# Performance work log

Measured on AMD Instinct MI355X. Metric: run time of the kernel, lower is better.

The kernel has to match this reference:

```python
import jax, jax.numpy as jnp
import numpy as np

EPS = 1e-12  # torch F.normalize default eps

def _l2norm(x, axis=-1):
    n = jnp.sqrt(jnp.sum(x * x, axis=axis, keepdims=True))
    return x / jnp.maximum(n, EPS)

def setup_inputs() -> dict:
    key = jax.random.key(0)
    k1, k2, k3 = jax.random.split(key, 3)
    B, L, D, C, J = 16, 1024, 768, 500, 10
    spatial = jax.random.normal(k1, (B, L, D), dtype=jnp.float32)
    prototypes = jax.random.normal(k2, (C, J, D), dtype=jnp.float32) * 0.02
    raw_weights = jnp.full((C, J), -2.0, dtype=jnp.float32) + 0.1 * jax.random.normal(k3, (C, J), dtype=jnp.float32)
    bias = jnp.zeros((C,), dtype=jnp.float32)
    return {"spatial": spatial, "prototypes": prototypes, "raw_weights": raw_weights, "bias": bias}

def reference(spatial, prototypes, raw_weights, bias):
    # spatial: (B, L, D); prototypes: (C, J, D)
    z = _l2norm(spatial)            # (B, L, D)
    p = _l2norm(prototypes)         # (C, J, D)
    sim = jnp.einsum('bld,cjd->blcj', z, p)   # (B, L, C, J)
    pooled = jnp.max(sim, axis=1)              # (B, C, J) max over L
    weights = jax.nn.softplus(raw_weights)     # (C, J)
    logits = jnp.sum(pooled * weights[None], axis=-1) + bias  # (B, C)
    return logits
```

## Files before the change

### kernel.cpp

```cpp
#include <hip/hip_runtime.h>

#define B_     16
#define L_     1024
#define D_     768
#define C_     500
#define J_     10
#define M_     (B_ * L_)
#define NREAL  (C_ * J_)
#define NPAD   5120
#define TM     256
#define TN     256
#define TK     64
#define KTILES (D_ / TK)

typedef __attribute__((ext_vector_type(8))) short short8;
typedef __attribute__((ext_vector_type(4))) float f32x4;

struct frag2 { short8 k[2]; };

static __device__ __forceinline__ unsigned f2ord(float f) {
    unsigned u = __float_as_uint(f);
    return (u & 0x80000000u) ? ~u : (u | 0x80000000u);
}
static __device__ __forceinline__ float ord2f(unsigned u) {
    return (u & 0x80000000u) ? __uint_as_float(u & 0x7fffffffu)
                             : __uint_as_float(~u);
}

static __device__ __forceinline__ unsigned short f2bf(float f) {
    unsigned u = __float_as_uint(f);
    u += 0x7fffu + ((u >> 16) & 1u);
    return (unsigned short)(u >> 16);
}

__global__ __launch_bounds__(256) void prep_kernel(
    const float* __restrict__ spatial, const float* __restrict__ protos,
    unsigned short* __restrict__ z, unsigned short* __restrict__ pbuf,
    unsigned int* __restrict__ pooled)
{
    const int bid = blockIdx.x;
    if (bid < 80) {
        uint4 zz = {0, 0, 0, 0};
        *(uint4*)(pooled + bid * 1024 + threadIdx.x * 4) = zz;
    }

    const float* in;
    unsigned short* out;
    int row, valid;
    if (bid < 4096) { in = spatial; out = z;    row = bid * 4 + (threadIdx.x >> 6);          valid = M_; }
    else            { in = protos;  out = pbuf; row = (bid - 4096) * 4 + (threadIdx.x >> 6); valid = NREAL; }
    const int lane = threadIdx.x & 63;

    unsigned short* orow = out + (size_t)row * D_;
    if (row >= valid) {
        ushort4 zz = {0, 0, 0, 0};
        #pragma unroll
        for (int p = 0; p < 3; ++p)
            *(ushort4*)(orow + (p * 64 + lane) * 4) = zz;
        return;
    }

    const float4* rp = (const float4*)(in + (size_t)row * D_);
    float4 v[3];
    float s = 0.f;
    #pragma unroll
    for (int p = 0; p < 3; ++p) {
        v[p] = rp[p * 64 + lane];
        s += v[p].x * v[p].x + v[p].y * v[p].y + v[p].z * v[p].z + v[p].w * v[p].w;
    }
    #pragma unroll
    for (int off = 32; off; off >>= 1) s += __shfl_xor(s, off);
    float inv = 1.f / fmaxf(sqrtf(s), 1e-12f);
    #pragma unroll
    for (int p = 0; p < 3; ++p) {
        ushort4 o;
        o.x = f2bf(v[p].x * inv);
        o.y = f2bf(v[p].y * inv);
        o.z = f2bf(v[p].z * inv);
        o.w = f2bf(v[p].w * inv);
        *(ushort4*)(orow + (p * 64 + lane) * 4) = o;
    }
}


#define MFMA(a, b, c) __builtin_amdgcn_mfma_f32_16x16x32_bf16(a, b, c, 0, 0, 0)
#define FENCE asm volatile("" ::: "memory")
#define BAR   do { FENCE; __builtin_amdgcn_s_barrier(); FENCE; } while (0)
#define VM(N) asm volatile("s_waitcnt vmcnt(" #N ")" ::: "memory")
#define PRIO1 __builtin_amdgcn_s_setprio(1)
#define PRIO0 __builtin_amdgcn_s_setprio(0)

#define RD_A2(dst, p, mi) do { \
    dst[0].k[0] = *(const short8*)(bA0 + (p)*32768 + (mi)*1024); \
    dst[0].k[1] = *(const short8*)(bA1 + (p)*32768 + (mi)*1024); \
    dst[1].k[0] = *(const short8*)(bA0 + (p)*32768 + ((mi)+1)*1024); \
    dst[1].k[1] = *(const short8*)(bA1 + (p)*32768 + ((mi)+1)*1024); \
} while (0)

#define RD_B4(dst, p) do { \
    _Pragma("unroll") \
    for (int ni_ = 0; ni_ < 4; ++ni_) { \
        dst[ni_].k[0] = *(const short8*)(bB0 + (p)*32768 + ni_*1024); \
        dst[ni_].k[1] = *(const short8*)(bB1 + (p)*32768 + ni_*1024); \
    } \
} while (0)

#define STAGE_A(p, q, k0) __builtin_amdgcn_global_load_lds( \
    (const __attribute__((address_space(1))) void*)(Z + gA0 + (q)*64*D_ + (unsigned)(k0)), \
    (__attribute__((address_space(3))) void*)(lds + (p)*32768 + (q)*4096 + tid8), 16, 0, 0)
#define STAGE_B(p, q, k0) __builtin_amdgcn_global_load_lds( \
    (const __attribute__((address_space(1))) void*)(Pm + gB0 + (q)*64*D_ + (unsigned)(k0)), \
    (__attribute__((address_space(3))) void*)(lds + (p)*32768 + 16384 + (q)*4096 + tid8), 16, 0, 0)

#define MMPAIR(j, S, Bv) do { \
    PRIO1; \
    _Pragma("unroll") \
    for (int ni_ = 0; ni_ < 4; ++ni_) { \
        acc[2*(j)][ni_]   = MFMA(S[0].k[0], Bv[ni_].k[0], acc[2*(j)][ni_]); \
        acc[2*(j)+1][ni_] = MFMA(S[1].k[0], Bv[ni_].k[0], acc[2*(j)+1][ni_]); \
        acc[2*(j)][ni_]   = MFMA(S[0].k[1], Bv[ni_].k[1], acc[2*(j)][ni_]); \
        acc[2*(j)+1][ni_] = MFMA(S[1].k[1], Bv[ni_].k[1], acc[2*(j)+1][ni_]); \
    } \
    PRIO0; \
} while (0)

__global__ __launch_bounds__(512, 1) void gemm_maxpool_kernel(
    const unsigned short* __restrict__ Z,
    const unsigned short* __restrict__ Pm,
    unsigned int* __restrict__ pooled)
{
    __shared__ unsigned short lds[65536];

    const int tid  = threadIdx.x;
    const int lane = tid & 63;
    const int wid  = tid >> 6;
    const int wm   = wid >> 2;
    const int wn   = wid & 3;

    const int xcd = (int)blockIdx.x & 7;
    const int idx = (int)blockIdx.x >> 3;
    const int bm  = xcd * 8 + (idx & 7);
    const int bn  = idx >> 3;
    const int row0 = bm * TM;
    const int col0 = bn * TN;

    const int tr    = tid >> 3;
    const int tswz  = ((tid & 7) * 16) ^ ((tr & 7) << 4);
    const int tid8  = tid * 8;
    const unsigned gA0 = (unsigned)(row0 + tr) * D_ + (tswz >> 1);
    const unsigned gB0 = (unsigned)(col0 + tr) * D_ + (tswz >> 1);

    const int l15   = lane & 15;
    const int swzl  = (lane & 7) << 4;
    const int colS0 = ((((lane >> 4) * 16)      ) ^ swzl) >> 1;
    const int colS1 = ((((lane >> 4) * 16) + 64 ) ^ swzl) >> 1;
    const unsigned short* bA0 = lds + (wm * 128 + l15) * 64 + colS0;
    const unsigned short* bA1 = lds + (wm * 128 + l15) * 64 + colS1;
    const unsigned short* bB0 = lds + 16384 + (wn * 64 + l15) * 64 + colS0;
    const unsigned short* bB1 = lds + 16384 + (wn * 64 + l15) * 64 + colS1;

    f32x4 acc[8][4] = {};
    frag2 aE[2], aO[2], bE[4], bO[4];

    STAGE_B(0,0,0);  STAGE_B(0,1,0);  STAGE_A(0,0,0);  STAGE_A(0,2,0);
    STAGE_B(0,2,0);  STAGE_B(0,3,0);  STAGE_A(0,1,0);  STAGE_A(0,3,0);
    STAGE_B(1,0,64); STAGE_B(1,1,64); STAGE_A(1,0,64); STAGE_A(1,2,64);
    STAGE_B(1,2,64); STAGE_B(1,3,64); STAGE_A(1,1,64); STAGE_A(1,3,64);
    VM(8);
    BAR;
    RD_B4(bE, 0);
    RD_A2(aE, 0, 0);

    #pragma unroll 1
    for (int i = 0; i < 5; ++i) {
        const int kE = i * 128 + 128;
        const int kO = i * 128 + 192;
        frag2 t23[2], t45[2], t67[2];

        RD_A2(t23, 0, 2);  STAGE_B(0, 0, kE);  STAGE_B(0, 1, kE);
        BAR; MMPAIR(0, aE, bE); BAR;

        RD_A2(t45, 0, 4);  STAGE_A(0, 0, kE);  STAGE_A(0, 2, kE);
        BAR; MMPAIR(1, t23, bE); BAR;

        RD_A2(t67, 0, 6);  STAGE_B(0, 2, kE);  STAGE_B(0, 3, kE);
        VM(6);
        BAR; MMPAIR(2, t45, bE); BAR;

        STAGE_A(0, 1, kE);  STAGE_A(0, 3, kE);
        MMPAIR(3, t67, bE);
        RD_B4(bO, 1);  RD_A2(aO, 1, 0);
        BAR;

        RD_A2(t23, 1, 2);  STAGE_B(1, 0, kO);  STAGE_B(1, 1, kO);
        BAR; MMPAIR(0, aO, bO); BAR;

        RD_A2(t45, 1, 4);  STAGE_A(1, 0, kO);  STAGE_A(1, 2, kO);
        BAR; MMPAIR(1, t23, bO); BAR;

        RD_A2(t67, 1, 6);  STAGE_B(1, 2, kO);  STAGE_B(1, 3, kO);
        VM(6);
        BAR; MMPAIR(2, t45, bO); BAR;

        STAGE_A(1, 1, kO);  STAGE_A(1, 3, kO);
        MMPAIR(3, t67, bO);
        RD_B4(bE, 0);  RD_A2(aE, 0, 0);
        BAR;
    }

    {
        frag2 t23[2], t45[2], t67[2];
        RD_A2(t23, 0, 2);
        BAR; MMPAIR(0, aE, bE); BAR;
        RD_A2(t45, 0, 4);
        BAR; MMPAIR(1, t23, bE); BAR;
        RD_A2(t67, 0, 6);
        VM(0);
        BAR; MMPAIR(2, t45, bE); BAR;
        MMPAIR(3, t67, bE);
        RD_B4(bO, 1);  RD_A2(aO, 1, 0);
        BAR;

        RD_A2(t23, 1, 2);
        BAR; MMPAIR(0, aO, bO); BAR;
        RD_A2(t45, 1, 4);
        BAR; MMPAIR(1, t23, bO); BAR;
        RD_A2(t67, 1, 6);
        BAR; MMPAIR(2, t45, bO); BAR;
        MMPAIR(3, t67, bO);
    }

    const int batch = row0 >> 10;
    #pragma unroll
    for (int ni = 0; ni < 4; ++ni) {
        float v = -3.0e38f;
        #pragma unroll
        for (int mi = 0; mi < 8; ++mi)
            v = fmaxf(v, fmaxf(fmaxf(acc[mi][ni][0], acc[mi][ni][1]),
                               fmaxf(acc[mi][ni][2], acc[mi][ni][3])));
        v = fmaxf(v, __shfl_xor(v, 16));
        v = fmaxf(v, __shfl_xor(v, 32));
        if (lane < 16) {
            int col = col0 + wn * 64 + ni * 16 + lane;
            atomicMax(&pooled[(size_t)batch * NPAD + col], f2ord(v));
        }
    }
}

__global__ __launch_bounds__(256) void finalize_kernel(
    const unsigned int* __restrict__ pooled,
    const float* __restrict__ rw,
    const float* __restrict__ bias,
    float* __restrict__ out)
{
    int t = blockIdx.x * 256 + threadIdx.x;
    if (t >= B_ * C_) return;
    int b = t / C_, c = t % C_;
    float s = 0.f;
    #pragma unroll
    for (int j = 0; j < J_; ++j) {
        float pv = ord2f(pooled[(size_t)b * NPAD + c * J_ + j]);
        float x  = rw[c * J_ + j];
        float w  = fmaxf(x, 0.f) + log1pf(expf(-fabsf(x)));
        s += pv * w;
    }
    out[t] = s + bias[c];
}

extern "C" void kernel_launch(void* const* d_in, const int* in_sizes, int n_in,
                              void* d_out, int out_size, void* d_ws, size_t ws_size,
                              hipStream_t stream) {
    const float* spatial = (const float*)d_in[0];
    const float* protos  = (const float*)d_in[1];
    const float* rw      = (const float*)d_in[2];
    const float* bias    = (const float*)d_in[3];
    float* out = (float*)d_out;

    unsigned short* z = (unsigned short*)d_ws;
    unsigned short* p = z + (size_t)M_ * D_;
    unsigned int* pooled = (unsigned int*)(p + (size_t)NPAD * D_);

    prep_kernel<<<M_ / 4 + NPAD / 4, 256, 0, stream>>>(spatial, protos, z, p, pooled);
    gemm_maxpool_kernel<<<(M_ / TM) * (NPAD / TN), 512, 0, stream>>>(z, p, pooled);
    finalize_kernel<<<(B_ * C_ + 255) / 256, 256, 0, stream>>>(pooled, rw, bias, out);
}
```

Baseline: 118.1 us.

## Reschedule global-to-LDS staging and drop barrier after each MFMA block

Moves the last two A-tile stages of the odd buffer into the next iteration's first phase, so each phase's loads shift by one slot, and relaxes the vmcnt waits from 6 to 4. It also removes the barrier that followed each MFMA pair, so LDS reads, global stages and MFMAs can overlap more freely within a wave. The aim is to cut barrier stalls and to hide global-load latency. The risk is LDS races, since stores into buffers may now be ordered against other waves' reads by fewer barriers. The reordered waits could also be wrong.

Result: no change. 116.3 us (-1.6%).

```diff
diff --git a/kernel.cpp b/kernel.cpp
--- a/kernel.cpp
+++ b/kernel.cpp
@@ -165,44 +165,45 @@
     STAGE_B(0,0,0);  STAGE_B(0,1,0);  STAGE_A(0,0,0);  STAGE_A(0,2,0);
     STAGE_B(0,2,0);  STAGE_B(0,3,0);  STAGE_A(0,1,0);  STAGE_A(0,3,0);
     STAGE_B(1,0,64); STAGE_B(1,1,64); STAGE_A(1,0,64); STAGE_A(1,2,64);
-    STAGE_B(1,2,64); STAGE_B(1,3,64); STAGE_A(1,1,64); STAGE_A(1,3,64);
-    VM(8);
+    STAGE_B(1,2,64); STAGE_B(1,3,64);
+    VM(6);
     BAR;
     RD_B4(bE, 0);
     RD_A2(aE, 0, 0);
 
     #pragma unroll 1
     for (int i = 0; i < 5; ++i) {
-        const int kE = i * 128 + 128;
-        const int kO = i * 128 + 192;
+        const int kOp = i * 128 + 64;
+        const int kE  = i * 128 + 128;
+        const int kO  = i * 128 + 192;
         frag2 t23[2], t45[2], t67[2];
 
-        RD_A2(t23, 0, 2);  STAGE_B(0, 0, kE);  STAGE_B(0, 1, kE);
-        BAR; MMPAIR(0, aE, bE); BAR;
-
-        RD_A2(t45, 0, 4);  STAGE_A(0, 0, kE);  STAGE_A(0, 2, kE);
-        BAR; MMPAIR(1, t23, bE); BAR;
-
-        RD_A2(t67, 0, 6);  STAGE_B(0, 2, kE);  STAGE_B(0, 3, kE);
-        VM(6);
-        BAR; MMPAIR(2, t45, bE); BAR;
-
-        STAGE_A(0, 1, kE);  STAGE_A(0, 3, kE);
+        RD_A2(t23, 0, 2);  STAGE_A(1, 1, kOp);  STAGE_A(1, 3, kOp);
+        BAR; MMPAIR(0, aE, bE);
+
+        RD_A2(t45, 0, 4);  STAGE_B(0, 0, kE);  STAGE_B(0, 1, kE);
+        BAR; MMPAIR(1, t23, bE);
+
+        RD_A2(t67, 0, 6);  STAGE_A(0, 0, kE);  STAGE_A(0, 2, kE);
+        VM(4);
+        BAR; MMPAIR(2, t45, bE);
+
+        STAGE_B(0, 2, kE);  STAGE_B(0, 3, kE);
         MMPAIR(3, t67, bE);
         RD_B4(bO, 1);  RD_A2(aO, 1, 0);
         BAR;
 
-        RD_A2(t23, 1, 2);  STAGE_B(1, 0, kO);  STAGE_B(1, 1, kO);
-        BAR; MMPAIR(0, aO, bO); BAR;
-
-        RD_A2(t45, 1, 4);  STAGE_A(1, 0, kO);  STAGE_A(1, 2, kO);
-        BAR; MMPAIR(1, t23, bO); BAR;
-
-        RD_A2(t67, 1, 6);  STAGE_B(1, 2, kO);  STAGE_B(1, 3, kO);
-        VM(6);
-        BAR; MMPAIR(2, t45, bO); BAR;
-
-        STAGE_A(1, 1, kO);  STAGE_A(1, 3, kO);
+        RD_A2(t23, 1, 2);  STAGE_A(0, 1, kE);  STAGE_A(0, 3, kE);
+        BAR; MMPAIR(0, aO, bO);
+
+        RD_A2(t45, 1, 4);  STAGE_B(1, 0, kO);  STAGE_B(1, 1, kO);
+        BAR; MMPAIR(1, t23, bO);
+
+        RD_A2(t67, 1, 6);  STAGE_A(1, 0, kO);  STAGE_A(1, 2, kO);
+        VM(4);
+        BAR; MMPAIR(2, t45, bO);
+
+        STAGE_B(1, 2, kO);  STAGE_B(1, 3, kO);
         MMPAIR(3, t67, bO);
         RD_B4(bE, 0);  RD_A2(aE, 0, 0);
         BAR;
@@ -210,23 +211,29 @@
 
     {
         frag2 t23[2], t45[2], t67[2];
-        RD_A2(t23, 0, 2);
-        BAR; MMPAIR(0, aE, bE); BAR;
+        RD_A2(t23, 0, 2);  STAGE_A(1, 1, 704);  STAGE_A(1, 3, 704);
+        BAR; MMPAIR(0, aE, bE);
+
         RD_A2(t45, 0, 4);
-        BAR; MMPAIR(1, t23, bE); BAR;
+        BAR; MMPAIR(1, t23, bE);
+
         RD_A2(t67, 0, 6);
         VM(0);
-        BAR; MMPAIR(2, t45, bE); BAR;
+        BAR; MMPAIR(2, t45, bE);
+
         MMPAIR(3, t67, bE);
         RD_B4(bO, 1);  RD_A2(aO, 1, 0);
         BAR;
 
         RD_A2(t23, 1, 2);
-        BAR; MMPAIR(0, aO, bO); BAR;
+        BAR; MMPAIR(0, aO, bO);
+
         RD_A2(t45, 1, 4);
-        BAR; MMPAIR(1, t23, bO); BAR;
+        BAR; MMPAIR(1, t23, bO);
+
         RD_A2(t67, 1, 6);
-        BAR; MMPAIR(2, t45, bO); BAR;
+        BAR; MMPAIR(2, t45, bO);
+
         MMPAIR(3, t67, bO);
     }
 
```
